# Kernel tuning notes

Measured on AMD Instinct MI355X. Metric: run time of the kernel, lower is better.

## Reference

```python
import jax, jax.numpy as jnp
import numpy as np

NEG_INF = -1e9  # mask fill value used by the original module


def setup_inputs() -> dict:
    key = jax.random.key(0)
    k1, k2, k3 = jax.random.split(key, 3)
    B, S, D, DQK = 4, 4096, 1024, 64
    encodings = jax.random.normal(k1, (B, S, D), dtype=jnp.float32)
    # nn.Linear weight layout: [out_features, in_features]
    W_q = jax.random.normal(k2, (DQK, D), dtype=jnp.float32) * (1.0 / np.sqrt(D))
    W_k = jax.random.normal(k3, (DQK, D), dtype=jnp.float32) * (1.0 / np.sqrt(D))
    return {"encodings": encodings, "W_q": W_q, "W_k": W_k}


def reference(encodings, W_q, W_k):
    # q, k: [B, S, d_qk]
    q = jnp.einsum('bsd,ed->bse', encodings, W_q)
    k = jnp.einsum('bsd,ed->bse', encodings, W_k)
    d_qk = k.shape[-1]
    # scores: [B, S, S]
    sims = jnp.einsum('bqe,bke->bqk', q, k) / jnp.sqrt(jnp.float32(d_qk))
    S = encodings.shape[1]
    # causal mask: mask strictly-upper triangle (future positions)
    causal = jnp.triu(jnp.ones((S, S), dtype=bool), k=1)
    sims = jnp.where(causal[None, :, :], jnp.float32(NEG_INF), sims)
    attn = jax.nn.softmax(sims, axis=-1)
    # values are the raw encodings (no W_v in this module)
    return jnp.einsum('bqk,bkd->bqd', attn, encodings)
```

## Files before the change

kernel.cpp:

```cpp
#include <hip/hip_runtime.h>

typedef __bf16 bf16;
typedef bf16 bf16x8 __attribute__((ext_vector_type(8)));
typedef float f32x4 __attribute__((ext_vector_type(4)));
typedef unsigned int u32;
typedef unsigned short u16;

#define BB 4
#define SS 4096
#define DD 1024
#define EE 64
static constexpr float SCALE2 = 0.18033688011112042f;
static constexpr float MFIX = 16.0f;

#define MFMA(a,b,c) __builtin_amdgcn_mfma_f32_16x16x32_bf16((a),(b),(c),0,0,0)

typedef __attribute__((address_space(3))) unsigned int lds_u32;
typedef const __attribute__((address_space(1))) unsigned int glb_u32;

static __device__ __forceinline__ void gload16(const void* g, void* l) {
    __builtin_amdgcn_global_load_lds((glb_u32*)g, (lds_u32*)l, 16, 0, 0);
}

static __device__ __forceinline__ u16 f2bf(float x) {
    union { float f; u32 u; } v; v.f = x;
    u32 r = v.u + 0x7FFFu + ((v.u >> 16) & 1u);
    return (u16)(r >> 16);
}
static __device__ __forceinline__ u32 pk2(float a, float b) {
    return (u32)f2bf(a) | ((u32)f2bf(b) << 16);
}
static __device__ __forceinline__ float fexp2(float x) {
    return __builtin_amdgcn_exp2f(x);
}

__global__ __launch_bounds__(512, 4) void k_proj(const float* __restrict__ enc,
                                                 const float* __restrict__ wq,
                                                 const float* __restrict__ wk,
                                                 u16* __restrict__ qout,
                                                 u16* __restrict__ kout) {
    __shared__ __align__(16) u16 la[64 * 64];
    __shared__ __align__(16) u16 lw[128 * 64];
    const int tid = threadIdx.x;
    const int m0 = blockIdx.x * 64;
    const int w = tid >> 6, lane = tid & 63, l15 = lane & 15, quad = lane >> 4;
    const int ari = tid >> 3, ag = tid & 7;
    const int wri = tid >> 2, wg = (tid & 3) * 2;
    const float* arow = enc + (size_t)(m0 + ari) * DD + ag * 8;
    const float* wrow = ((wri < 64) ? (wq + (size_t)wri * DD) : (wk + (size_t)(wri - 64) * DD)) + (tid & 3) * 16;

    float4 a0 = *(const float4*)(arow);
    float4 a1 = *(const float4*)(arow + 4);
    float4 b0 = *(const float4*)(wrow);
    float4 b1 = *(const float4*)(wrow + 4);
    float4 b2 = *(const float4*)(wrow + 8);
    float4 b3 = *(const float4*)(wrow + 12);

    f32x4 acc[4];
#pragma unroll
    for (int i = 0; i < 4; i++) acc[i] = f32x4{0.f, 0.f, 0.f, 0.f};

    for (int kk = 0; kk < DD; kk += 64) {
        uint4 pa, pw0, pw1;
        pa.x = pk2(a0.x, a0.y); pa.y = pk2(a0.z, a0.w);
        pa.z = pk2(a1.x, a1.y); pa.w = pk2(a1.z, a1.w);
        pw0.x = pk2(b0.x, b0.y); pw0.y = pk2(b0.z, b0.w);
        pw0.z = pk2(b1.x, b1.y); pw0.w = pk2(b1.z, b1.w);
        pw1.x = pk2(b2.x, b2.y); pw1.y = pk2(b2.z, b2.w);
        pw1.z = pk2(b3.x, b3.y); pw1.w = pk2(b3.z, b3.w);
        __syncthreads();
        *(uint4*)&la[ari * 64 + (ag ^ (ari & 7)) * 8] = pa;
        *(uint4*)&lw[wri * 64 + ((wg + 0) ^ (wri & 7)) * 8] = pw0;
        *(uint4*)&lw[wri * 64 + ((wg + 1) ^ (wri & 7)) * 8] = pw1;
        __syncthreads();
        if (kk + 64 < DD) {
            a0 = *(const float4*)(arow + kk + 64);
            a1 = *(const float4*)(arow + kk + 68);
            b0 = *(const float4*)(wrow + kk + 64);
            b1 = *(const float4*)(wrow + kk + 68);
            b2 = *(const float4*)(wrow + kk + 72);
            b3 = *(const float4*)(wrow + kk + 76);
        }
        int m = 16 * (w & 3) + l15;
#pragma unroll
        for (int es = 0; es < 2; es++) {
            bf16x8 af = *(const bf16x8*)&la[m * 64 + ((((es << 2) + quad) ^ (m & 7))) * 8];
#pragma unroll
            for (int ct = 0; ct < 4; ct++) {
                int n = 64 * (w >> 2) + 16 * ct + l15;
                bf16x8 bf_ = *(const bf16x8*)&lw[n * 64 + ((((es << 2) + quad) ^ (n & 7))) * 8];
                acc[ct] = MFMA(af, bf_, acc[ct]);
            }
        }
    }
#pragma unroll
    for (int ct = 0; ct < 4; ct++) {
        int n = 64 * (w >> 2) + 16 * ct + l15;
        u16* dst = (n < 64) ? qout : kout;
        int col = n & 63;
#pragma unroll
        for (int r = 0; r < 4; r++) {
            int grow = m0 + 16 * (w & 3) + 4 * quad + r;
            dst[(size_t)grow * EE + col] = f2bf(acc[ct][r]);
        }
    }
}

__global__ __launch_bounds__(256) void k_tcast(const float* __restrict__ enc, u16* __restrict__ vt) {
    __shared__ u32 lt2[32][67];
    const int tid = threadIdx.x;
    const int dt = blockIdx.x, st = blockIdx.y, b = blockIdx.z;
    const int srow = tid >> 2, d0 = (tid & 3) << 4;
    const float* src = enc + ((size_t)(b * SS + st * 64 + srow) * DD) + dt * 64 + d0;
    float4 f0 = ((const float4*)src)[0];
    float4 f1 = ((const float4*)src)[1];
    float4 f2 = ((const float4*)src)[2];
    float4 f3 = ((const float4*)src)[3];
    float v[16];
    v[0] = f0.x; v[1] = f0.y; v[2] = f0.z; v[3] = f0.w;
    v[4] = f1.x; v[5] = f1.y; v[6] = f1.z; v[7] = f1.w;
    v[8] = f2.x; v[9] = f2.y; v[10] = f2.z; v[11] = f2.w;
    v[12] = f3.x; v[13] = f3.y; v[14] = f3.z; v[15] = f3.w;
#pragma unroll
    for (int j = 0; j < 8; j++) lt2[(d0 >> 1) + j][srow] = pk2(v[2 * j], v[2 * j + 1]);
    __syncthreads();
    const int dp = tid >> 3, soct = tid & 7;
    u32 a[8];
#pragma unroll
    for (int j = 0; j < 8; j++) a[j] = lt2[dp][soct * 8 + j];
    uint4 r0, r1;
    r0.x = (a[0] & 0xffffu) | (a[1] << 16);
    r0.y = (a[2] & 0xffffu) | (a[3] << 16);
    r0.z = (a[4] & 0xffffu) | (a[5] << 16);
    r0.w = (a[6] & 0xffffu) | (a[7] << 16);
    r1.x = (a[0] >> 16) | (a[1] & 0xffff0000u);
    r1.y = (a[2] >> 16) | (a[3] & 0xffff0000u);
    r1.z = (a[4] >> 16) | (a[5] & 0xffff0000u);
    r1.w = (a[6] >> 16) | (a[7] & 0xffff0000u);
    u16* dst0 = vt + ((size_t)(b * DD + dt * 64 + 2 * dp) * SS) + st * 64 + soct * 8;
    *(uint4*)dst0 = r0;
    *(uint4*)(dst0 + SS) = r1;
}

__global__ __launch_bounds__(512, 2) void k_attn(const u16* __restrict__ qg, const u16* __restrict__ kg,
                                                 const u16* __restrict__ vt, float* __restrict__ out) {
    __shared__ __align__(16) u16 lds[49408];
    u16* lp = lds;
    float* lsum = (float*)&lds[8192];
    const int tid = threadIdx.x;
    const int w = tid >> 6, lane = tid & 63, l15 = lane & 15, quad = lane >> 4;
    const int pr = blockIdx.x & 15, combo = blockIdx.x >> 4;
    const int ds = combo & 3, b = combo >> 2;
    const int d0 = ds * 256;
    const int kr = w & 1, qc = w >> 1;
    const int dc = w & 3, qr = w >> 2;
    const u16* kbase = kg + (size_t)b * SS * EE;
    const u16* vbase = vt + ((size_t)b * DD + d0) * SS;

    for (int half = 0; half < 2; half++) {
        const int qt = half ? pr : (31 - pr);
        const int q0 = qt * 128;
        const int KT = 2 * qt + 2;
        const u16* qbase = qg + ((size_t)b * SS + q0) * EE;
        __syncthreads();
        if (tid < 128) lsum[tid] = 0.f;
        {
            int goff = tid, grow = goff >> 3, glog = (goff & 7) ^ (grow & 7);
            gload16(kbase + (size_t)grow * EE + glog * 8, (void*)&lds[8448 + goff * 8]);
#pragma unroll
            for (int i = 0; i < 4; i++) {
                int go = i * 512 + tid, gr = go >> 3, gl = (go & 7) ^ (gr & 7);
                gload16(vbase + (size_t)gr * SS + gl * 8, (void*)&lds[8448 + 4096 + go * 8]);
            }
        }
        bf16x8 qf[2][2];
#pragma unroll
        for (int ct = 0; ct < 2; ct++) {
            int qv = 32 * qc + 16 * ct + l15;
#pragma unroll
            for (int es = 0; es < 2; es++)
                qf[ct][es] = *(const bf16x8*)(qbase + (size_t)qv * EE + es * 32 + quad * 8);
        }
        f32x4 o[4][4];
#pragma unroll
        for (int i = 0; i < 4; i++)
#pragma unroll
            for (int j = 0; j < 4; j++) o[i][j] = f32x4{0.f, 0.f, 0.f, 0.f};
        float rl[2] = {0.f, 0.f};
        __syncthreads();

        for (int kt = 0; kt < KT; kt++) {
            const int k0 = kt * 64;
            const u16* lk = &lds[8448 + (kt & 1) * 20480];
            const u16* lv = lk + 4096;
            const bool dg = (kt >= KT - 2);
#pragma unroll
            for (int rt = 0; rt < 2; rt++) {
                int m = 32 * kr + 16 * rt + l15;
                bf16x8 ka0 = *(const bf16x8*)&lk[m * 64 + ((quad ^ (m & 7))) * 8];
                bf16x8 ka1 = *(const bf16x8*)&lk[m * 64 + (((4 + quad) ^ (m & 7))) * 8];
#pragma unroll
                for (int ct = 0; ct < 2; ct++) {
                    f32x4 c = f32x4{0.f, 0.f, 0.f, 0.f};
                    c = MFMA(ka0, qf[ct][0], c);
                    c = MFMA(ka1, qf[ct][1], c);
                    int qv = 32 * qc + 16 * ct + l15;
                    float p[4];
#pragma unroll
                    for (int r = 0; r < 4; r++) {
                        float arg = __builtin_fmaf(c[r], SCALE2, -MFIX);
                        if (dg) {
                            int kp = k0 + 32 * kr + 16 * rt + 4 * quad + r;
                            if (kp > q0 + qv) arg = -3.0e38f;
                        }
                        p[r] = fexp2(arg);
                    }
                    rl[ct] += (p[0] + p[1]) + (p[2] + p[3]);
                    int g16 = 4 * kr + 2 * rt + (quad >> 1);
                    uint2 pkk;
                    pkk.x = pk2(p[0], p[1]);
                    pkk.y = pk2(p[2], p[3]);
                    *(uint2*)&lp[qv * 64 + (g16 ^ (qv & 7)) * 8 + (quad & 1) * 4] = pkk;
                }
            }
            __syncthreads();
            if (kt + 1 < KT) {
                int k1 = k0 + 64;
                u16* nb = &lds[8448 + ((kt + 1) & 1) * 20480];
                int goff = tid, grow = goff >> 3, glog = (goff & 7) ^ (grow & 7);
                gload16(kbase + (size_t)(k1 + grow) * EE + glog * 8, (void*)&nb[goff * 8]);
#pragma unroll
                for (int i = 0; i < 4; i++) {
                    int go = i * 512 + tid, gr = go >> 3, gl = (go & 7) ^ (gr & 7);
                    gload16(vbase + (size_t)gr * SS + k1 + gl * 8, (void*)&nb[4096 + go * 8]);
                }
            }
#pragma unroll
            for (int ks = 0; ks < 2; ks++) {
                bf16x8 vb[4];
#pragma unroll
                for (int ct = 0; ct < 4; ct++) {
                    int n = 64 * dc + 16 * ct + l15;
                    vb[ct] = *(const bf16x8*)&lv[n * 64 + ((((ks << 2) + quad) ^ (n & 7))) * 8];
                }
#pragma unroll
                for (int rt = 0; rt < 4; rt++) {
                    int m = 64 * qr + 16 * rt + l15;
                    bf16x8 pa = *(const bf16x8*)&lp[m * 64 + ((((ks << 2) + quad) ^ (m & 7))) * 8];
#pragma unroll
                    for (int ct = 0; ct < 4; ct++) o[rt][ct] = MFMA(pa, vb[ct], o[rt][ct]);
                }
            }
            __syncthreads();
        }
#pragma unroll
        for (int ct = 0; ct < 2; ct++) {
            float t = rl[ct];
            t += __shfl_xor(t, 16, 64);
            t += __shfl_xor(t, 32, 64);
            if (quad == 0) atomicAdd(&lsum[32 * qc + 16 * ct + l15], t);
        }
        __syncthreads();
        float* obase = out + ((size_t)b * SS + q0) * DD + d0 + dc * 64;
#pragma unroll
        for (int rt = 0; rt < 4; rt++) {
#pragma unroll
            for (int r = 0; r < 4; r++) {
                int row = 64 * qr + 16 * rt + 4 * quad + r;
                float li = 1.0f / lsum[row];
#pragma unroll
                for (int ct = 0; ct < 4; ct++)
                    obase[(size_t)row * DD + ct * 16 + l15] = o[rt][ct][r] * li;
            }
        }
    }
}

extern "C" void kernel_launch(void* const* d_in, const int* in_sizes, int n_in,
                              void* d_out, int out_size, void* d_ws, size_t ws_size,
                              hipStream_t stream) {
    (void)in_sizes; (void)n_in; (void)out_size; (void)ws_size;
    const float* enc = (const float*)d_in[0];
    const float* wq = (const float*)d_in[1];
    const float* wk = (const float*)d_in[2];
    char* ws = (char*)d_ws;
    u16* qbf = (u16*)ws;
    u16* kbf = (u16*)(ws + (2ull << 20));
    u16* vt  = (u16*)(ws + (4ull << 20));
    float* out = (float*)d_out;

    hipLaunchKernelGGL(k_proj, dim3(256), dim3(512), 0, stream, enc, wq, wk, qbf, kbf);
    hipLaunchKernelGGL(k_tcast, dim3(16, 64, 4), dim3(256), 0, stream, enc, vt);
    hipLaunchKernelGGL(k_attn, dim3(256), dim3(512), 0, stream, qbf, kbf, vt, out);
}
```

Measured before the change: 255.8 us.

## Merge projection and transpose kernels; prefetch K/V tiles through registers

Combines the Q/K projection and the V transpose-cast into one launch: the first 256 blocks do the projection and the remaining blocks each do two transpose tiles with 512 threads. In the attention loop, the next K/V tile is now fetched into registers before the QK^T compute and written to LDS after the barrier, replacing the direct global-to-LDS loads issued after the barrier. This removes one kernel launch and lets the global load latency overlap the score computation. The cost is extra registers and explicit LDS stores, which may lower occupancy under the 2-blocks launch bound.

```diff
diff --git a/kernel.cpp b/kernel.cpp
--- a/kernel.cpp
+++ b/kernel.cpp
@@ -34,112 +34,116 @@
     return __builtin_amdgcn_exp2f(x);
 }
 
-__global__ __launch_bounds__(512, 4) void k_proj(const float* __restrict__ enc,
+__global__ __launch_bounds__(512, 4) void k_prep(const float* __restrict__ enc,
                                                  const float* __restrict__ wq,
                                                  const float* __restrict__ wk,
                                                  u16* __restrict__ qout,
-                                                 u16* __restrict__ kout) {
-    __shared__ __align__(16) u16 la[64 * 64];
-    __shared__ __align__(16) u16 lw[128 * 64];
+                                                 u16* __restrict__ kout,
+                                                 u16* __restrict__ vt) {
+    __shared__ __align__(16) u16 sm[12288];
     const int tid = threadIdx.x;
-    const int m0 = blockIdx.x * 64;
-    const int w = tid >> 6, lane = tid & 63, l15 = lane & 15, quad = lane >> 4;
-    const int ari = tid >> 3, ag = tid & 7;
-    const int wri = tid >> 2, wg = (tid & 3) * 2;
-    const float* arow = enc + (size_t)(m0 + ari) * DD + ag * 8;
-    const float* wrow = ((wri < 64) ? (wq + (size_t)wri * DD) : (wk + (size_t)(wri - 64) * DD)) + (tid & 3) * 16;
-
-    float4 a0 = *(const float4*)(arow);
-    float4 a1 = *(const float4*)(arow + 4);
-    float4 b0 = *(const float4*)(wrow);
-    float4 b1 = *(const float4*)(wrow + 4);
-    float4 b2 = *(const float4*)(wrow + 8);
-    float4 b3 = *(const float4*)(wrow + 12);
-
-    f32x4 acc[4];
-#pragma unroll
-    for (int i = 0; i < 4; i++) acc[i] = f32x4{0.f, 0.f, 0.f, 0.f};
-
-    for (int kk = 0; kk < DD; kk += 64) {
-        uint4 pa, pw0, pw1;
-        pa.x = pk2(a0.x, a0.y); pa.y = pk2(a0.z, a0.w);
-        pa.z = pk2(a1.x, a1.y); pa.w = pk2(a1.z, a1.w);
-        pw0.x = pk2(b0.x, b0.y); pw0.y = pk2(b0.z, b0.w);
-        pw0.z = pk2(b1.x, b1.y); pw0.w = pk2(b1.z, b1.w);
-        pw1.x = pk2(b2.x, b2.y); pw1.y = pk2(b2.z, b2.w);
-        pw1.z = pk2(b3.x, b3.y); pw1.w = pk2(b3.z, b3.w);
+    if (blockIdx.x < 256) {
+        u16* la = sm;
+        u16* lw = sm + 4096;
+        const int m0 = blockIdx.x * 64;
+        const int w = tid >> 6, lane = tid & 63, l15 = lane & 15, quad = lane >> 4;
+        const int ari = tid >> 3, ag = tid & 7;
+        const int wri = tid >> 2, wg = (tid & 3) * 2;
+        const float* arow = enc + (size_t)(m0 + ari) * DD + ag * 8;
+        const float* wrow = ((wri < 64) ? (wq + (size_t)wri * DD) : (wk + (size_t)(wri - 64) * DD)) + (tid & 3) * 16;
+
+        float4 a0 = *(const float4*)(arow);
+        float4 a1 = *(const float4*)(arow + 4);
+        float4 b0 = *(const float4*)(wrow);
+        float4 b1 = *(const float4*)(wrow + 4);
+        float4 b2 = *(const float4*)(wrow + 8);
+        float4 b3 = *(const float4*)(wrow + 12);
+
+        f32x4 acc[4];
+#pragma unroll
+        for (int i = 0; i < 4; i++) acc[i] = f32x4{0.f, 0.f, 0.f, 0.f};
+
+        for (int kk = 0; kk < DD; kk += 64) {
+            uint4 pa, pw0, pw1;
+            pa.x = pk2(a0.x, a0.y); pa.y = pk2(a0.z, a0.w);
+            pa.z = pk2(a1.x, a1.y); pa.w = pk2(a1.z, a1.w);
+            pw0.x = pk2(b0.x, b0.y); pw0.y = pk2(b0.z, b0.w);
+            pw0.z = pk2(b1.x, b1.y); pw0.w = pk2(b1.z, b1.w);
+            pw1.x = pk2(b2.x, b2.y); pw1.y = pk2(b2.z, b2.w);
+            pw1.z = pk2(b3.x, b3.y); pw1.w = pk2(b3.z, b3.w);
+            __syncthreads();
+            *(uint4*)&la[ari * 64 + (ag ^ (ari & 7)) * 8] = pa;
+            *(uint4*)&lw[wri * 64 + ((wg + 0) ^ (wri & 7)) * 8] = pw0;
+            *(uint4*)&lw[wri * 64 + ((wg + 1) ^ (wri & 7)) * 8] = pw1;
+            __syncthreads();
+            if (kk + 64 < DD) {
+                a0 = *(const float4*)(arow + kk + 64);
+                a1 = *(const float4*)(arow + kk + 68);
+                b0 = *(const float4*)(wrow + kk + 64);
+                b1 = *(const float4*)(wrow + kk + 68);
+                b2 = *(const float4*)(wrow + kk + 72);
+                b3 = *(const float4*)(wrow + kk + 76);
+            }
+            int m = 16 * (w & 3) + l15;
+#pragma unroll
+            for (int es = 0; es < 2; es++) {
+                bf16x8 af = *(const bf16x8*)&la[m * 64 + ((((es << 2) + quad) ^ (m & 7))) * 8];
+#pragma unroll
+                for (int ct = 0; ct < 4; ct++) {
+                    int n = 64 * (w >> 2) + 16 * ct + l15;
+                    bf16x8 bf_ = *(const bf16x8*)&lw[n * 64 + ((((es << 2) + quad) ^ (n & 7))) * 8];
+                    acc[ct] = MFMA(af, bf_, acc[ct]);
+                }
+            }
+        }
+#pragma unroll
+        for (int ct = 0; ct < 4; ct++) {
+            int n = 64 * (w >> 2) + 16 * ct + l15;
+            u16* dst = (n < 64) ? qout : kout;
+            int col = n & 63;
+#pragma unroll
+            for (int r = 0; r < 4; r++) {
+                int grow = m0 + 16 * (w & 3) + 4 * quad + r;
+                dst[(size_t)grow * EE + col] = f2bf(acc[ct][r]);
+            }
+        }
+    } else {
+        u32* lt2 = (u32*)sm + (tid >> 8) * 2144;
+        const int t = tid & 255;
+        const int tc = blockIdx.x - 256;
+        const int dt = tc & 15, stp = (tc >> 4) & 31, b = tc >> 9;
+        const int st = stp * 2 + (tid >> 8);
+        const int srow = t >> 2, d0 = (t & 3) << 4;
+        const float* src = enc + ((size_t)(b * SS + st * 64 + srow) * DD) + dt * 64 + d0;
+        float4 f0 = ((const float4*)src)[0];
+        float4 f1 = ((const float4*)src)[1];
+        float4 f2 = ((const float4*)src)[2];
+        float4 f3 = ((const float4*)src)[3];
+        float v[16];
+        v[0] = f0.x; v[1] = f0.y; v[2] = f0.z; v[3] = f0.w;
+        v[4] = f1.x; v[5] = f1.y; v[6] = f1.z; v[7] = f1.w;
+        v[8] = f2.x; v[9] = f2.y; v[10] = f2.z; v[11] = f2.w;
+        v[12] = f3.x; v[13] = f3.y; v[14] = f3.z; v[15] = f3.w;
+#pragma unroll
+        for (int j = 0; j < 8; j++) lt2[((d0 >> 1) + j) * 67 + srow] = pk2(v[2 * j], v[2 * j + 1]);
         __syncthreads();
-        *(uint4*)&la[ari * 64 + (ag ^ (ari & 7)) * 8] = pa;
-        *(uint4*)&lw[wri * 64 + ((wg + 0) ^ (wri & 7)) * 8] = pw0;
-        *(uint4*)&lw[wri * 64 + ((wg + 1) ^ (wri & 7)) * 8] = pw1;
-        __syncthreads();
-        if (kk + 64 < DD) {
-            a0 = *(const float4*)(arow + kk + 64);
-            a1 = *(const float4*)(arow + kk + 68);
-            b0 = *(const float4*)(wrow + kk + 64);
-            b1 = *(const float4*)(wrow + kk + 68);
-            b2 = *(const float4*)(wrow + kk + 72);
-            b3 = *(const float4*)(wrow + kk + 76);
-        }
-        int m = 16 * (w & 3) + l15;
-#pragma unroll
-        for (int es = 0; es < 2; es++) {
-            bf16x8 af = *(const bf16x8*)&la[m * 64 + ((((es << 2) + quad) ^ (m & 7))) * 8];
-#pragma unroll
-            for (int ct = 0; ct < 4; ct++) {
-                int n = 64 * (w >> 2) + 16 * ct + l15;
-                bf16x8 bf_ = *(const bf16x8*)&lw[n * 64 + ((((es << 2) + quad) ^ (n & 7))) * 8];
-                acc[ct] = MFMA(af, bf_, acc[ct]);
-            }
-        }
+        const int dp = t >> 3, soct = t & 7;
+        u32 a[8];
+#pragma unroll
+        for (int j = 0; j < 8; j++) a[j] = lt2[dp * 67 + soct * 8 + j];
+        uint4 r0, r1;
+        r0.x = (a[0] & 0xffffu) | (a[1] << 16);
+        r0.y = (a[2] & 0xffffu) | (a[3] << 16);
+        r0.z = (a[4] & 0xffffu) | (a[5] << 16);
+        r0.w = (a[6] & 0xffffu) | (a[7] << 16);
+        r1.x = (a[0] >> 16) | (a[1] & 0xffff0000u);
+        r1.y = (a[2] >> 16) | (a[3] & 0xffff0000u);
+        r1.z = (a[4] >> 16) | (a[5] & 0xffff0000u);
+        r1.w = (a[6] >> 16) | (a[7] & 0xffff0000u);
+        u16* dst0 = vt + ((size_t)(b * DD + dt * 64 + 2 * dp) * SS) + st * 64 + soct * 8;
+        *(uint4*)dst0 = r0;
+        *(uint4*)(dst0 + SS) = r1;
     }
-#pragma unroll
-    for (int ct = 0; ct < 4; ct++) {
-        int n = 64 * (w >> 2) + 16 * ct + l15;
-        u16* dst = (n < 64) ? qout : kout;
-        int col = n & 63;
-#pragma unroll
-        for (int r = 0; r < 4; r++) {
-            int grow = m0 + 16 * (w & 3) + 4 * quad + r;
-            dst[(size_t)grow * EE + col] = f2bf(acc[ct][r]);
-        }
-    }
-}
-
-__global__ __launch_bounds__(256) void k_tcast(const float* __restrict__ enc, u16* __restrict__ vt) {
-    __shared__ u32 lt2[32][67];
-    const int tid = threadIdx.x;
-    const int dt = blockIdx.x, st = blockIdx.y, b = blockIdx.z;
-    const int srow = tid >> 2, d0 = (tid & 3) << 4;
-    const float* src = enc + ((size_t)(b * SS + st * 64 + srow) * DD) + dt * 64 + d0;
-    float4 f0 = ((const float4*)src)[0];
-    float4 f1 = ((const float4*)src)[1];
-    float4 f2 = ((const float4*)src)[2];
-    float4 f3 = ((const float4*)src)[3];
-    float v[16];
-    v[0] = f0.x; v[1] = f0.y; v[2] = f0.z; v[3] = f0.w;
-    v[4] = f1.x; v[5] = f1.y; v[6] = f1.z; v[7] = f1.w;
-    v[8] = f2.x; v[9] = f2.y; v[10] = f2.z; v[11] = f2.w;
-    v[12] = f3.x; v[13] = f3.y; v[14] = f3.z; v[15] = f3.w;
-#pragma unroll
-    for (int j = 0; j < 8; j++) lt2[(d0 >> 1) + j][srow] = pk2(v[2 * j], v[2 * j + 1]);
-    __syncthreads();
-    const int dp = tid >> 3, soct = tid & 7;
-    u32 a[8];
-#pragma unroll
-    for (int j = 0; j < 8; j++) a[j] = lt2[dp][soct * 8 + j];
-    uint4 r0, r1;
-    r0.x = (a[0] & 0xffffu) | (a[1] << 16);
-    r0.y = (a[2] & 0xffffu) | (a[3] << 16);
-    r0.z = (a[4] & 0xffffu) | (a[5] << 16);
-    r0.w = (a[6] & 0xffffu) | (a[7] << 16);
-    r1.x = (a[0] >> 16) | (a[1] & 0xffff0000u);
-    r1.y = (a[2] >> 16) | (a[3] & 0xffff0000u);
-    r1.z = (a[4] >> 16) | (a[5] & 0xffff0000u);
-    r1.w = (a[6] >> 16) | (a[7] & 0xffff0000u);
-    u16* dst0 = vt + ((size_t)(b * DD + dt * 64 + 2 * dp) * SS) + st * 64 + soct * 8;
-    *(uint4*)dst0 = r0;
-    *(uint4*)(dst0 + SS) = r1;
 }
 
 __global__ __launch_bounds__(512, 2) void k_attn(const u16* __restrict__ qg, const u16* __restrict__ kg,
@@ -157,6 +161,20 @@
     const u16* kbase = kg + (size_t)b * SS * EE;
     const u16* vbase = vt + ((size_t)b * DD + d0) * SS;
 
+    const int kgrow = tid >> 3, kglog = (tid & 7) ^ (kgrow & 7);
+    const u16* kptr = kbase + (size_t)kgrow * EE + kglog * 8;
+    const u16* vptr0; const u16* vptr1; const u16* vptr2; const u16* vptr3;
+    {
+        int go0 = 0 * 512 + tid, gr0 = go0 >> 3, gl0 = (go0 & 7) ^ (gr0 & 7);
+        int go1 = 1 * 512 + tid, gr1 = go1 >> 3, gl1 = (go1 & 7) ^ (gr1 & 7);
+        int go2 = 2 * 512 + tid, gr2 = go2 >> 3, gl2 = (go2 & 7) ^ (gr2 & 7);
+        int go3 = 3 * 512 + tid, gr3 = go3 >> 3, gl3 = (go3 & 7) ^ (gr3 & 7);
+        vptr0 = vbase + (size_t)gr0 * SS + gl0 * 8;
+        vptr1 = vbase + (size_t)gr1 * SS + gl1 * 8;
+        vptr2 = vbase + (size_t)gr2 * SS + gl2 * 8;
+        vptr3 = vbase + (size_t)gr3 * SS + gl3 * 8;
+    }
+
     for (int half = 0; half < 2; half++) {
         const int qt = half ? pr : (31 - pr);
         const int q0 = qt * 128;
@@ -194,6 +212,16 @@
             const u16* lk = &lds[8448 + (kt & 1) * 20480];
             const u16* lv = lk + 4096;
             const bool dg = (kt >= KT - 2);
+            const bool pf = (kt + 1 < KT);
+            uint4 gk, gv0, gv1, gv2, gv3;
+            if (pf) {
+                const int k1 = k0 + 64;
+                gk  = *(const uint4*)(kptr + (size_t)k1 * EE);
+                gv0 = *(const uint4*)(vptr0 + k1);
+                gv1 = *(const uint4*)(vptr1 + k1);
+                gv2 = *(const uint4*)(vptr2 + k1);
+                gv3 = *(const uint4*)(vptr3 + k1);
+            }
 #pragma unroll
             for (int rt = 0; rt < 2; rt++) {
                 int m = 32 * kr + 16 * rt + l15;
@@ -224,16 +252,13 @@
                 }
             }
             __syncthreads();
-            if (kt + 1 < KT) {
-                int k1 = k0 + 64;
+            if (pf) {
                 u16* nb = &lds[8448 + ((kt + 1) & 1) * 20480];
-                int goff = tid, grow = goff >> 3, glog = (goff & 7) ^ (grow & 7);
-                gload16(kbase + (size_t)(k1 + grow) * EE + glog * 8, (void*)&nb[goff * 8]);
-#pragma unroll
-                for (int i = 0; i < 4; i++) {
-                    int go = i * 512 + tid, gr = go >> 3, gl = (go & 7) ^ (gr & 7);
-                    gload16(vbase + (size_t)gr * SS + k1 + gl * 8, (void*)&nb[4096 + go * 8]);
-                }
+                *(uint4*)&nb[tid * 8] = gk;
+                *(uint4*)&nb[4096 + (0 * 512 + tid) * 8] = gv0;
+                *(uint4*)&nb[4096 + (1 * 512 + tid) * 8] = gv1;
+                *(uint4*)&nb[4096 + (2 * 512 + tid) * 8] = gv2;
+                *(uint4*)&nb[4096 + (3 * 512 + tid) * 8] = gv3;
             }
 #pragma unroll
             for (int ks = 0; ks < 2; ks++) {
@@ -289,7 +314,6 @@
     u16* vt  = (u16*)(ws + (4ull << 20));
     float* out = (float*)d_out;
 
-    hipLaunchKernelGGL(k_proj, dim3(256), dim3(512), 0, stream, enc, wq, wk, qbf, kbf);
-    hipLaunchKernelGGL(k_tcast, dim3(16, 64, 4), dim3(256), 0, stream, enc, vt);
+    hipLaunchKernelGGL(k_prep, dim3(2304), dim3(512), 0, stream, enc, wq, wk, qbf, kbf, vt);
     hipLaunchKernelGGL(k_attn, dim3(256), dim3(512), 0, stream, qbf, kbf, vt, out);
 }
```

Result: faster. 244.0 us (-4.6%).
